# Optimization experiments

Measured on AMD Instinct MI355X. Metric: run time of the kernel, lower is better.

Reference implementation:

```python
import jax, jax.numpy as jnp
import numpy as np

FEATURES = 1024
NUM_HEADS = 16
HEAD_DIM = FEATURES // NUM_HEADS


def _cinit(key, shape):
    # complex_xavier_init from the source: std = sqrt(1/(fan_in + fan_out))
    fan_in = int(np.prod(shape[:-1]))
    fan_out = shape[-1]
    std = np.sqrt(1.0 / (fan_in + fan_out)).astype(np.float32)
    return jax.random.normal(key, shape, dtype=jnp.float32) * std


def setup_inputs() -> dict:
    key = jax.random.key(0)
    ks = jax.random.split(key, 12)
    B, S, F = 2, 2048, FEATURES
    inp = {
        'x_r': jax.random.normal(ks[0], (B, S, F), dtype=jnp.float32),
        'x_i': jax.random.normal(ks[1], (B, S, F), dtype=jnp.float32),
        'mask': jnp.ones((B, S), dtype=jnp.float32),
    }
    names = ['q', 'k', 'v', 'o']
    for idx, n in enumerate(names):
        inp[f'W{n}_r'] = _cinit(ks[2 + 2 * idx], (F, F))
        inp[f'W{n}_i'] = _cinit(ks[3 + 2 * idx], (F, F))
        inp[f'b{n}_r'] = jnp.zeros((F,), dtype=jnp.float32)
        inp[f'b{n}_i'] = jnp.zeros((F,), dtype=jnp.float32)
    return inp


def _complex_linear(xr, xi, Wr, Wi, br, bi):
    # (xr + i xi) @ (Wr + i Wi) + (br + i bi)
    yr = xr @ Wr - xi @ Wi + br
    yi = xr @ Wi + xi @ Wr + bi
    return yr, yi


def reference(x_r, x_i, mask,
              Wq_r, Wq_i, bq_r, bq_i,
              Wk_r, Wk_i, bk_r, bk_i,
              Wv_r, Wv_i, bv_r, bv_i,
              Wo_r, Wo_i, bo_r, bo_i):
    B, S, F = x_r.shape
    H, D = NUM_HEADS, HEAD_DIM

    Qr, Qi = _complex_linear(x_r, x_i, Wq_r, Wq_i, bq_r, bq_i)
    Kr, Ki = _complex_linear(x_r, x_i, Wk_r, Wk_i, bk_r, bk_i)
    Vr, Vi = _complex_linear(x_r, x_i, Wv_r, Wv_i, bv_r, bv_i)

    def split_heads(t):  # [B,S,F] -> [B,H,S,D]
        return t.reshape(B, S, H, D).transpose(0, 2, 1, 3)

    Qr, Qi, Kr, Ki, Vr, Vi = map(split_heads, (Qr, Qi, Kr, Ki, Vr, Vi))

    scale = 1.0 / jnp.sqrt(jnp.float32(D))
    # Re(Q K^H) = Qr.Kr + Qi.Ki
    scores = (jnp.einsum('bhqd,bhkd->bhqk', Qr, Kr)
              + jnp.einsum('bhqd,bhkd->bhqk', Qi, Ki)) * scale
    scores = scores + (1.0 - mask[:, None, None, :]) * -1e9
    attn = jax.nn.softmax(scores, axis=-1)  # real-valued weights

    out_r = jnp.einsum('bhqk,bhkd->bhqd', attn, Vr)
    out_i = jnp.einsum('bhqk,bhkd->bhqd', attn, Vi)

    def merge_heads(t):  # [B,H,S,D] -> [B,S,F]
        return t.transpose(0, 2, 1, 3).reshape(B, S, F)

    out_r, out_i = merge_heads(out_r), merge_heads(out_i)
    out_r, out_i = _complex_linear(out_r, out_i, Wo_r, Wo_i, bo_r, bo_i)
    # stack real/imag parts: [2, B, S, F]
    return jnp.stack([out_r, out_i], axis=0)
```

## Files before the change

kernel.cpp:

```cpp
#include <hip/hip_runtime.h>
#include <hip/hip_bf16.h>

typedef unsigned short u16;
typedef unsigned int   u32;
typedef __attribute__((ext_vector_type(8))) short bf16x8;
typedef __attribute__((ext_vector_type(4))) float f32x4;

#define FDIM 1024
#define NH   16
#define HD   64
#define SEQ  2048

#define MFMA16 __builtin_amdgcn_mfma_f32_16x16x32_bf16

__device__ __forceinline__ u16 f2bf(float f) {
    __hip_bfloat16 h = __float2bfloat16(f);
    return *reinterpret_cast<u16*>(&h);
}

__device__ __forceinline__ void g2l16(const u16* g, u16* l) {
    __builtin_amdgcn_global_load_lds(
        (const __attribute__((address_space(1))) unsigned int*)g,
        (__attribute__((address_space(3))) unsigned int*)l,
        16, 0, 0);
}

__global__ __launch_bounds__(256)
void convert_x(const float* __restrict__ xr, const float* __restrict__ xi,
               u16* __restrict__ dr, u16* __restrict__ di)
{
    const long n4 = (long)2 * SEQ * FDIM / 4;
    for (long i = (long)blockIdx.x * blockDim.x + threadIdx.x; i < n4;
         i += (long)gridDim.x * blockDim.x) {
        float4 v = ((const float4*)xr)[i];
        ushort4 o;
        o.x = f2bf(v.x); o.y = f2bf(v.y); o.z = f2bf(v.z); o.w = f2bf(v.w);
        ((ushort4*)dr)[i] = o;
        v = ((const float4*)xi)[i];
        o.x = f2bf(v.x); o.y = f2bf(v.y); o.z = f2bf(v.z); o.w = f2bf(v.w);
        ((ushort4*)di)[i] = o;
    }
}

__global__ __launch_bounds__(256)
void convert_w(const float* __restrict__ W0, const float* __restrict__ W1,
               const float* __restrict__ W2, const float* __restrict__ W3,
               const float* __restrict__ W4, const float* __restrict__ W5,
               const float* __restrict__ W6, const float* __restrict__ W7,
               u16* __restrict__ wt_base)
{
    __shared__ u16 T[64][68];
    const int z = blockIdx.z;
    const float* W = (z == 0) ? W0 : (z == 1) ? W1 : (z == 2) ? W2 : (z == 3) ? W3
                   : (z == 4) ? W4 : (z == 5) ? W5 : (z == 6) ? W6 : W7;
    u16* Wt = wt_base + (long)z * FDIM * FDIM;
    const int n0 = blockIdx.x * 64, k0 = blockIdx.y * 64;
    const int tid = threadIdx.x;
    const int cr = tid & 15, rr = tid >> 4;
    #pragma unroll
    for (int p = 0; p < 4; p++) {
        const int k = p * 16 + rr;
        float4 v = *(const float4*)&W[(long)(k0 + k) * FDIM + n0 + cr * 4];
        T[k][cr*4 + 0] = f2bf(v.x); T[k][cr*4 + 1] = f2bf(v.y);
        T[k][cr*4 + 2] = f2bf(v.z); T[k][cr*4 + 3] = f2bf(v.w);
    }
    __syncthreads();
    #pragma unroll
    for (int p = 0; p < 4; p++) {
        const int n = p * 16 + rr;
        ushort4 o;
        o.x = T[cr*4 + 0][n]; o.y = T[cr*4 + 1][n];
        o.z = T[cr*4 + 2][n]; o.w = T[cr*4 + 3][n];
        *(ushort4*)&Wt[(long)(n0 + n) * FDIM + k0 + cr*4] = o;
    }
}

__global__ __launch_bounds__(256, 3)
void proj_bf16(const u16* __restrict__ Xr_g, const u16* __restrict__ Xi_g,
               const u16* __restrict__ Wt_base,
               const float* __restrict__ bqr, const float* __restrict__ bqi,
               const float* __restrict__ bkr, const float* __restrict__ bki,
               const float* __restrict__ bvr, const float* __restrict__ bvi,
               u16* __restrict__ ws)
{
    __shared__ u16 XsR[2][64 * 32],  XsI[2][64 * 32];
    __shared__ u16 WsR[2][128 * 32], WsI[2][128 * 32];

    const int z = blockIdx.z, t = z % 3, b = z / 3;
    const u16* xr = Xr_g + (long)b * SEQ * FDIM;
    const u16* xi = Xi_g + (long)b * SEQ * FDIM;
    const long WT = (long)FDIM * FDIM;
    const u16* wr = Wt_base + (long)(2 * t) * WT;
    const u16* wi = wr + WT;
    const float* br = (t == 0) ? bqr : (t == 1) ? bkr : bvr;
    const float* bi = (t == 0) ? bqi : (t == 1) ? bki : bvi;
    const long TS = (long)2 * SEQ * FDIM;
    u16* outR = ws + (long)(t * 2) * TS + (long)b * SEQ * FDIM;
    u16* outI = outR + TS;

    const int tid = threadIdx.x;
    const int n0  = blockIdx.x * 128;
    const int m0  = blockIdx.y * 64;

    const int lane = tid & 63;
    const int wv   = tid >> 6;
    const int mwo  = (wv >> 1) * 32;
    const int nwo  = (wv & 1) * 64;
    const int ml   = lane & 15;
    const int kg   = lane >> 4;

    const int lr = lane >> 2;
    const int xc = (((lane & 3) ^ (lr & 3)) * 8);
    const int rc = ((kg ^ (ml & 3)) * 8);

    f32x4 accr[2][4], acci[2][4];
    #pragma unroll
    for (int i = 0; i < 2; i++)
        #pragma unroll
        for (int j = 0; j < 4; j++) { accr[i][j] = (f32x4)(0.0f); acci[i][j] = (f32x4)(0.0f); }

    #define PSTAGE(bufi, kk)                                                     \
        do {                                                                     \
            const int rsx  = wv * 16;                                            \
            const int rowx = rsx + lr;                                           \
            g2l16(xr + (long)(m0 + rowx) * FDIM + (kk) + xc, &XsR[bufi][rsx * 32]); \
            g2l16(xi + (long)(m0 + rowx) * FDIM + (kk) + xc, &XsI[bufi][rsx * 32]); \
            _Pragma("unroll")                                                    \
            for (int sub = 0; sub < 2; sub++) {                                  \
                const int rs  = wv * 32 + sub * 16;                              \
                const int row = rs + lr;                                         \
                g2l16(wr + (long)(n0 + row) * FDIM + (kk) + xc, &WsR[bufi][rs * 32]); \
                g2l16(wi + (long)(n0 + row) * FDIM + (kk) + xc, &WsI[bufi][rs * 32]); \
            }                                                                    \
        } while (0)

    int buf = 0;
    PSTAGE(0, 0);
    __syncthreads();

    for (int k0 = 0; k0 < FDIM; k0 += 32) {
        if (k0 + 32 < FDIM) PSTAGE(buf ^ 1, k0 + 32);

        bf16x8 ar[2], ai[2], nai[2], brf[4], bif[4];
        #pragma unroll
        for (int i = 0; i < 2; i++) {
            ar[i] = *(const bf16x8*)&XsR[buf][(mwo + 16*i + ml) * 32 + rc];
            union { bf16x8 v; u32 w[4]; } u;
            u.v = *(const bf16x8*)&XsI[buf][(mwo + 16*i + ml) * 32 + rc];
            ai[i] = u.v;
            u.w[0] ^= 0x80008000u; u.w[1] ^= 0x80008000u;
            u.w[2] ^= 0x80008000u; u.w[3] ^= 0x80008000u;
            nai[i] = u.v;
        }
        #pragma unroll
        for (int j = 0; j < 4; j++) {
            brf[j] = *(const bf16x8*)&WsR[buf][(nwo + 16*j + ml) * 32 + rc];
            bif[j] = *(const bf16x8*)&WsI[buf][(nwo + 16*j + ml) * 32 + rc];
        }
        #pragma unroll
        for (int i = 0; i < 2; i++)
            #pragma unroll
            for (int j = 0; j < 4; j++) {
                accr[i][j] = MFMA16(ar[i],  brf[j], accr[i][j], 0, 0, 0);
                accr[i][j] = MFMA16(nai[i], bif[j], accr[i][j], 0, 0, 0);
                acci[i][j] = MFMA16(ar[i],  bif[j], acci[i][j], 0, 0, 0);
                acci[i][j] = MFMA16(ai[i],  brf[j], acci[i][j], 0, 0, 0);
            }

        __syncthreads();
        buf ^= 1;
    }
    #undef PSTAGE

    #pragma unroll
    for (int j = 0; j < 4; j++) {
        const int n = n0 + nwo + 16*j + ml;
        const int hh = n >> 6, d = n & 63;
        const float bre = br[n];
        const float bim = bi[n];
        #pragma unroll
        for (int i = 0; i < 2; i++) {
            const int mb = m0 + mwo + 16*i + kg*4;
            if (t < 2) {
                #pragma unroll
                for (int r = 0; r < 4; r++) {
                    const long addr = ((long)hh * SEQ + (mb + r)) * HD + d;
                    outR[addr] = f2bf(accr[i][j][r] + bre);
                    outI[addr] = f2bf(acci[i][j][r] + bim);
                }
            } else {
                const long addr = ((long)hh * HD + d) * SEQ + mb;
                ushort4 vr, vi;
                vr.x = f2bf(accr[i][j][0] + bre); vr.y = f2bf(accr[i][j][1] + bre);
                vr.z = f2bf(accr[i][j][2] + bre); vr.w = f2bf(accr[i][j][3] + bre);
                vi.x = f2bf(acci[i][j][0] + bim); vi.y = f2bf(acci[i][j][1] + bim);
                vi.z = f2bf(acci[i][j][2] + bim); vi.w = f2bf(acci[i][j][3] + bim);
                *(ushort4*)&outR[addr] = vr;
                *(ushort4*)&outI[addr] = vi;
            }
        }
    }
}

__global__ __launch_bounds__(256, 4)
void attn_mfma(const u16* __restrict__ Qr_g, const u16* __restrict__ Qi_g,
               const u16* __restrict__ Kr_g, const u16* __restrict__ Ki_g,
               const u16* __restrict__ Vtr_g, const u16* __restrict__ Vti_g,
               const float* __restrict__ mask_g,
               u16* __restrict__ Ar_g, u16* __restrict__ Ai_g)
{
    __shared__ u16 KT[64 * 128];
    __shared__ u16 VT[128 * 64];

    const int tid  = threadIdx.x;
    const int lane = tid & 63;
    const int wv   = tid >> 6;
    const int ml   = lane & 15;
    const int quad = lane >> 4;

    const int L   = blockIdx.x + (blockIdx.y << 5) + (blockIdx.z << 9);
    const int xcd = L & 7, qq = L >> 3;
    const int q0  = (qq & 31) * 64;
    const int g   = ((qq >> 5) << 3) | xcd;
    const int h   = g & 15;
    const int b   = g >> 4;
    const long hb  = ((long)b * NH + h) * SEQ * HD;
    const float* mask = mask_g + (long)b * SEQ;

    bf16x8 qf[4];
    {
        const long row = hb + (long)(q0 + wv*16 + ml) * HD;
        qf[0] = *(const bf16x8*)(Qr_g + row + quad*8);
        qf[1] = *(const bf16x8*)(Qr_g + row + 32 + quad*8);
        qf[2] = *(const bf16x8*)(Qi_g + row + quad*8);
        qf[3] = *(const bf16x8*)(Qi_g + row + 32 + quad*8);
    }

    const u16* srcK[4];
    #pragma unroll
    for (int ii = 0; ii < 4; ii++) {
        const int rk = wv*16 + ii*4 + (lane >> 4);
        const int c  = (lane & 15) ^ (rk & 7);
        srcK[ii] = ((c < 8) ? Kr_g : Ki_g) + hb + (long)rk * HD + (c & 7) * 8;
    }
    const u16* srcV[4];
    #pragma unroll
    for (int jj = 0; jj < 4; jj++) {
        const int dv = wv*32 + jj*8 + (lane >> 3);
        const int c  = (lane & 7) ^ (dv & 7);
        srcV[jj] = ((dv < 64) ? Vtr_g : Vti_g) + hb + (long)(dv & 63) * SEQ + c * 8;
    }

    #define STAGE()                                                             \
        do {                                                                    \
            _Pragma("unroll")                                                   \
            for (int ii = 0; ii < 4; ii++)                                      \
                g2l16(srcK[ii], &KT[(wv*16 + ii*4) * 128]);                     \
            _Pragma("unroll")                                                   \
            for (int jj = 0; jj < 4; jj++)                                      \
                g2l16(srcV[jj], &VT[(wv*32 + jj*8) * 64]);                      \
            _Pragma("unroll")                                                   \
            for (int ii = 0; ii < 4; ii++) srcK[ii] += 64 * HD;                 \
            _Pragma("unroll")                                                   \
            for (int jj = 0; jj < 4; jj++) srcV[jj] += 64;                      \
        } while (0)

    f32x4 oacc[8];
    #pragma unroll
    for (int nt = 0; nt < 8; nt++) oacc[nt] = (f32x4)(0.0f);
    float m_run = -3.0e38f;
    float l_run = 0.0f;
    const float scale = 0.125f;

    const int NT = SEQ / 64;
    for (int t = 0; t < NT; ++t) {
        if (t) __syncthreads();
        STAGE();

        f32x4 mrow[4];
        #pragma unroll
        for (int mt = 0; mt < 4; mt++)
            mrow[mt] = *(const f32x4*)(mask + t*64 + mt*16 + quad*4);

        __syncthreads();

        f32x4 sacc[4];
        #pragma unroll
        for (int mt = 0; mt < 4; mt++) sacc[mt] = (f32x4)(0.0f);
        __builtin_amdgcn_s_setprio(1);
        #pragma unroll
        for (int mt = 0; mt < 4; mt++)
            #pragma unroll
            for (int kc = 0; kc < 4; kc++) {
                const bf16x8 kf = *(const bf16x8*)
                    &KT[(mt*16 + ml) * 128 + (((kc*4 + quad) ^ (ml & 7)) * 8)];
                sacc[mt] = MFMA16(kf, qf[kc], sacc[mt], 0, 0, 0);
            }
        __builtin_amdgcn_s_setprio(0);

        asm volatile("s_barrier" ::: "memory");

        u16* Pb = (u16*)&KT[0];
        float sv[4][4];
        #pragma unroll
        for (int mt = 0; mt < 4; mt++)
            #pragma unroll
            for (int r = 0; r < 4; r++)
                sv[mt][r] = sacc[mt][r] * scale + (1.0f - mrow[mt][r]) * -1.0e9f;

        float mA = fmaxf(fmaxf(sv[0][0], sv[0][1]), fmaxf(sv[0][2], sv[0][3]));
        float mB = fmaxf(fmaxf(sv[1][0], sv[1][1]), fmaxf(sv[1][2], sv[1][3]));
        float mC = fmaxf(fmaxf(sv[2][0], sv[2][1]), fmaxf(sv[2][2], sv[2][3]));
        float mD = fmaxf(fmaxf(sv[3][0], sv[3][1]), fmaxf(sv[3][2], sv[3][3]));
        float mx = fmaxf(fmaxf(mA, mB), fmaxf(mC, mD));
        mx = fmaxf(mx, __shfl_xor(mx, 16));
        mx = fmaxf(mx, __shfl_xor(mx, 32));
        const float mn = fmaxf(m_run, mx);
        const float al = __expf(m_run - mn);

        float p[4][4];
        #pragma unroll
        for (int mt = 0; mt < 4; mt++) {
            p[mt][0] = __expf(sv[mt][0] - mn);
            p[mt][1] = __expf(sv[mt][1] - mn);
            p[mt][2] = __expf(sv[mt][2] - mn);
            p[mt][3] = __expf(sv[mt][3] - mn);
        }
        const int qrow = wv*16 + ml;
        #pragma unroll
        for (int mt = 0; mt < 4; mt++) {
            ushort4 pb;
            pb.x = f2bf(p[mt][0]); pb.y = f2bf(p[mt][1]);
            pb.z = f2bf(p[mt][2]); pb.w = f2bf(p[mt][3]);
            *(ushort4*)&Pb[(long)qrow * 64
                           + (((mt*2 + (quad >> 1)) ^ (ml & 7)) * 8)
                           + (quad & 1) * 4] = pb;
        }
        float s0 = (p[0][0] + p[0][1]) + (p[0][2] + p[0][3]);
        float s1 = (p[1][0] + p[1][1]) + (p[1][2] + p[1][3]);
        float s2 = (p[2][0] + p[2][1]) + (p[2][2] + p[2][3]);
        float s3 = (p[3][0] + p[3][1]) + (p[3][2] + p[3][3]);
        float ps = (s0 + s1) + (s2 + s3);
        ps += __shfl_xor(ps, 16);
        ps += __shfl_xor(ps, 32);
        l_run = l_run * al + ps;
        m_run = mn;

        f32x4 al4;
        #pragma unroll
        for (int r = 0; r < 4; r++)
            al4[r] = __shfl(al, quad*20 + r);
        #pragma unroll
        for (int nt = 0; nt < 8; nt++) oacc[nt] *= al4;

        __builtin_amdgcn_s_setprio(1);
        #pragma unroll
        for (int kc = 0; kc < 2; kc++) {
            const int pchunk = ((kc*4 + quad) ^ (ml & 7)) * 8;
            const bf16x8 pf = *(const bf16x8*)&Pb[(long)qrow * 64 + pchunk];
            #pragma unroll
            for (int nt = 0; nt < 8; nt++) {
                const bf16x8 vf = *(const bf16x8*)
                    &VT[(nt*16 + ml) * 64 + (((kc*4 + quad) ^ (ml & 7)) * 8)];
                oacc[nt] = MFMA16(pf, vf, oacc[nt], 0, 0, 0);
            }
        }
        __builtin_amdgcn_s_setprio(0);
    }
    #undef STAGE

    const float linv = 1.0f / l_run;
    f32x4 li;
    #pragma unroll
    for (int r = 0; r < 4; r++)
        li[r] = __shfl(linv, quad*20 + r);
    const long abase = (long)b * SEQ * FDIM;
    #pragma unroll
    for (int nt = 0; nt < 8; nt++) {
        const int dim = nt*16 + ml;
        u16* dst = ((dim < 64) ? Ar_g : Ai_g) + abase
                 + (long)(q0 + wv*16 + quad*4) * FDIM + h * HD + (dim & 63);
        #pragma unroll
        for (int r = 0; r < 4; r++)
            dst[(long)r * FDIM] = f2bf(oacc[nt][r] * li[r]);
    }
}

__global__ __launch_bounds__(256, 3)
void oproj_bf16(const u16* __restrict__ Ar_all, const u16* __restrict__ Ai_all,
                const u16* __restrict__ Wtor,
                const float* __restrict__ bor, const float* __restrict__ boi,
                float* __restrict__ out)
{
    __shared__ u16 XsR[2][64 * 32],  XsI[2][64 * 32];
    __shared__ u16 WsR[2][128 * 32], WsI[2][128 * 32];

    const int b = blockIdx.z;
    const u16* ar = Ar_all + (long)b * SEQ * FDIM;
    const u16* ai = Ai_all + (long)b * SEQ * FDIM;
    const u16* wr = Wtor;
    const u16* wi = Wtor + (long)FDIM * FDIM;
    float* outR = out + (long)b * SEQ * FDIM;
    float* outI = out + (long)2 * SEQ * FDIM + (long)b * SEQ * FDIM;

    const int tid = threadIdx.x;
    const int n0  = blockIdx.x * 128;
    const int m0  = blockIdx.y * 64;

    const int lane = tid & 63;
    const int wv   = tid >> 6;
    const int mwo  = (wv >> 1) * 32;
    const int nwo  = (wv & 1) * 64;
    const int ml   = lane & 15;
    const int kg   = lane >> 4;

    const int lr = lane >> 2;
    const int xc = (((lane & 3) ^ (lr & 3)) * 8);
    const int rc = ((kg ^ (ml & 3)) * 8);

    f32x4 accr[2][4], acci[2][4];
    #pragma unroll
    for (int i = 0; i < 2; i++)
        #pragma unroll
        for (int j = 0; j < 4; j++) { accr[i][j] = (f32x4)(0.0f); acci[i][j] = (f32x4)(0.0f); }

    #define OSTAGE(bufi, kk)                                                     \
        do {                                                                     \
            const int rsx  = wv * 16;                                            \
            const int rowx = rsx + lr;                                           \
            g2l16(ar + (long)(m0 + rowx) * FDIM + (kk) + xc, &XsR[bufi][rsx * 32]); \
            g2l16(ai + (long)(m0 + rowx) * FDIM + (kk) + xc, &XsI[bufi][rsx * 32]); \
            _Pragma("unroll")                                                    \
            for (int sub = 0; sub < 2; sub++) {                                  \
                const int rs  = wv * 32 + sub * 16;                              \
                const int row = rs + lr;                                         \
                g2l16(wr + (long)(n0 + row) * FDIM + (kk) + xc, &WsR[bufi][rs * 32]); \
                g2l16(wi + (long)(n0 + row) * FDIM + (kk) + xc, &WsI[bufi][rs * 32]); \
            }                                                                    \
        } while (0)

    int buf = 0;
    OSTAGE(0, 0);
    __syncthreads();

    for (int k0 = 0; k0 < FDIM; k0 += 32) {
        if (k0 + 32 < FDIM) OSTAGE(buf ^ 1, k0 + 32);

        bf16x8 arf[2], aif[2], naif[2], brf[4], bif[4];
        #pragma unroll
        for (int i = 0; i < 2; i++) {
            arf[i] = *(const bf16x8*)&XsR[buf][(mwo + 16*i + ml) * 32 + rc];
            union { bf16x8 v; u32 w[4]; } u;
            u.v = *(const bf16x8*)&XsI[buf][(mwo + 16*i + ml) * 32 + rc];
            aif[i] = u.v;
            u.w[0] ^= 0x80008000u; u.w[1] ^= 0x80008000u;
            u.w[2] ^= 0x80008000u; u.w[3] ^= 0x80008000u;
            naif[i] = u.v;
        }
        #pragma unroll
        for (int j = 0; j < 4; j++) {
            brf[j] = *(const bf16x8*)&WsR[buf][(nwo + 16*j + ml) * 32 + rc];
            bif[j] = *(const bf16x8*)&WsI[buf][(nwo + 16*j + ml) * 32 + rc];
        }
        #pragma unroll
        for (int i = 0; i < 2; i++)
            #pragma unroll
            for (int j = 0; j < 4; j++) {
                accr[i][j] = MFMA16(arf[i],  brf[j], accr[i][j], 0, 0, 0);
                accr[i][j] = MFMA16(naif[i], bif[j], accr[i][j], 0, 0, 0);
                acci[i][j] = MFMA16(arf[i],  bif[j], acci[i][j], 0, 0, 0);
                acci[i][j] = MFMA16(aif[i],  brf[j], acci[i][j], 0, 0, 0);
            }

        __syncthreads();
        buf ^= 1;
    }
    #undef OSTAGE

    #pragma unroll
    for (int j = 0; j < 4; j++) {
        const int n = n0 + nwo + 16*j + ml;
        const float bre = bor[n];
        const float bim = boi[n];
        #pragma unroll
        for (int i = 0; i < 2; i++) {
            #pragma unroll
            for (int r = 0; r < 4; r++) {
                const int m = m0 + mwo + 16*i + kg*4 + r;
                const long addr = (long)m * FDIM + n;
                outR[addr] = accr[i][j][r] + bre;
                outI[addr] = acci[i][j][r] + bim;
            }
        }
    }
}

extern "C" void kernel_launch(void* const* d_in, const int* in_sizes, int n_in,
                              void* d_out, int out_size, void* d_ws, size_t ws_size,
                              hipStream_t stream)
{
    const float* x_r  = (const float*)d_in[0];
    const float* x_i  = (const float*)d_in[1];
    const float* mask = (const float*)d_in[2];
    const float *Wq_r = (const float*)d_in[3],  *Wq_i = (const float*)d_in[4];
    const float *bq_r = (const float*)d_in[5],  *bq_i = (const float*)d_in[6];
    const float *Wk_r = (const float*)d_in[7],  *Wk_i = (const float*)d_in[8];
    const float *bk_r = (const float*)d_in[9],  *bk_i = (const float*)d_in[10];
    const float *Wv_r = (const float*)d_in[11], *Wv_i = (const float*)d_in[12];
    const float *bv_r = (const float*)d_in[13], *bv_i = (const float*)d_in[14];
    const float *Wo_r = (const float*)d_in[15], *Wo_i = (const float*)d_in[16];
    const float *bo_r = (const float*)d_in[17], *bo_i = (const float*)d_in[18];

    u16* ws = (u16*)d_ws;
    const long TS = (long)2 * SEQ * FDIM;
    const long WT = (long)FDIM * FDIM;
    u16 *Qr = ws,          *Qi = ws + TS;
    u16 *Kr = ws + 2*TS,   *Ki = ws + 3*TS;
    u16 *Vtr = ws + 4*TS,  *Vti = ws + 5*TS;
    u16 *Ar = ws + 6*TS,   *Ai = ws + 7*TS;
    u16 *Xbr = Ar,         *Xbi = Ai;
    u16 *Wt  = ws + 8*TS;

    convert_x<<<dim3(2048), 256, 0, stream>>>(x_r, x_i, Xbr, Xbi);
    convert_w<<<dim3(16, 16, 8), 256, 0, stream>>>(Wq_r, Wq_i, Wk_r, Wk_i,
                                                   Wv_r, Wv_i, Wo_r, Wo_i, Wt);

    proj_bf16<<<dim3(8, 32, 6), 256, 0, stream>>>(Xbr, Xbi, Wt,
        bq_r, bq_i, bk_r, bk_i, bv_r, bv_i, ws);

    attn_mfma<<<dim3(SEQ / 64, NH, 2), 256, 0, stream>>>(Qr, Qi, Kr, Ki, Vtr, Vti,
                                                         mask, Ar, Ai);

    oproj_bf16<<<dim3(8, 32, 2), 256, 0, stream>>>(Ar, Ai, Wt + 6*WT,
                                                   bo_r, bo_i, (float*)d_out);
}
```

Before: 392.8 us.

## Shrink projection tiles, remap blocks across XCDs, and use exp2 softmax with lazy rescale

The projection and output-projection GEMMs drop from 64x128 to 64x64 tiles, which doubles the grid, raises the occupancy hint to 4, and remaps block IDs so neighbouring N tiles land on the same XCD for L2 reuse. The attention softmax folds log2(e) into the scale, calls v_exp_f32 directly, and skips the accumulator rescale when no row max grows anywhere in the wave. Smaller tiles cut per-block data reuse and raise total global and LDS traffic, in exchange for more parallelism and better cache locality.

```diff
diff --git a/kernel.cpp b/kernel.cpp
--- a/kernel.cpp
+++ b/kernel.cpp
@@ -23,6 +23,12 @@
         (const __attribute__((address_space(1))) unsigned int*)g,
         (__attribute__((address_space(3))) unsigned int*)l,
         16, 0, 0);
+}
+
+__device__ __forceinline__ float exp2v(float x) {
+    float d;
+    asm("v_exp_f32 %0, %1" : "=v"(d) : "v"(x));
+    return d;
 }
 
 __global__ __launch_bounds__(256)
@@ -75,7 +81,7 @@
     }
 }
 
-__global__ __launch_bounds__(256, 3)
+__global__ __launch_bounds__(256, 4)
 void proj_bf16(const u16* __restrict__ Xr_g, const u16* __restrict__ Xi_g,
                const u16* __restrict__ Wt_base,
                const float* __restrict__ bqr, const float* __restrict__ bqi,
@@ -83,10 +89,19 @@
                const float* __restrict__ bvr, const float* __restrict__ bvi,
                u16* __restrict__ ws)
 {
-    __shared__ u16 XsR[2][64 * 32],  XsI[2][64 * 32];
-    __shared__ u16 WsR[2][128 * 32], WsI[2][128 * 32];
-
-    const int z = blockIdx.z, t = z % 3, b = z / 3;
+    __shared__ u16 XsR[2][64 * 32], XsI[2][64 * 32];
+    __shared__ u16 WsR[2][64 * 32], WsI[2][64 * 32];
+
+    const int L   = blockIdx.x + (blockIdx.y << 4) + (blockIdx.z << 9);
+    const int xcd = L & 7;
+    const int qq  = L >> 3;
+    const int y   = qq & 31;
+    const int gg  = qq >> 5;
+    const int gid = gg * 8 + xcd;
+    const int x   = gid & 15;
+    const int zz  = gid >> 4;
+    const int t = zz % 3, b = zz / 3;
+
     const u16* xr = Xr_g + (long)b * SEQ * FDIM;
     const u16* xi = Xi_g + (long)b * SEQ * FDIM;
     const long WT = (long)FDIM * FDIM;
@@ -99,13 +114,13 @@
     u16* outI = outR + TS;
 
     const int tid = threadIdx.x;
-    const int n0  = blockIdx.x * 128;
-    const int m0  = blockIdx.y * 64;
+    const int n0  = x * 64;
+    const int m0  = y * 64;
 
     const int lane = tid & 63;
     const int wv   = tid >> 6;
     const int mwo  = (wv >> 1) * 32;
-    const int nwo  = (wv & 1) * 64;
+    const int nwo  = (wv & 1) * 32;
     const int ml   = lane & 15;
     const int kg   = lane >> 4;
 
@@ -113,11 +128,11 @@
     const int xc = (((lane & 3) ^ (lr & 3)) * 8);
     const int rc = ((kg ^ (ml & 3)) * 8);
 
-    f32x4 accr[2][4], acci[2][4];
+    f32x4 accr[2][2], acci[2][2];
     #pragma unroll
     for (int i = 0; i < 2; i++)
         #pragma unroll
-        for (int j = 0; j < 4; j++) { accr[i][j] = (f32x4)(0.0f); acci[i][j] = (f32x4)(0.0f); }
+        for (int j = 0; j < 2; j++) { accr[i][j] = (f32x4)(0.0f); acci[i][j] = (f32x4)(0.0f); }
 
     #define PSTAGE(bufi, kk)                                                     \
         do {                                                                     \
@@ -125,13 +140,8 @@
             const int rowx = rsx + lr;                                           \
             g2l16(xr + (long)(m0 + rowx) * FDIM + (kk) + xc, &XsR[bufi][rsx * 32]); \
             g2l16(xi + (long)(m0 + rowx) * FDIM + (kk) + xc, &XsI[bufi][rsx * 32]); \
-            _Pragma("unroll")                                                    \
-            for (int sub = 0; sub < 2; sub++) {                                  \
-                const int rs  = wv * 32 + sub * 16;                              \
-                const int row = rs + lr;                                         \
-                g2l16(wr + (long)(n0 + row) * FDIM + (kk) + xc, &WsR[bufi][rs * 32]); \
-                g2l16(wi + (long)(n0 + row) * FDIM + (kk) + xc, &WsI[bufi][rs * 32]); \
-            }                                                                    \
+            g2l16(wr + (long)(n0 + rowx) * FDIM + (kk) + xc, &WsR[bufi][rsx * 32]); \
+            g2l16(wi + (long)(n0 + rowx) * FDIM + (kk) + xc, &WsI[bufi][rsx * 32]); \
         } while (0)
 
     int buf = 0;
@@ -141,7 +151,7 @@
     for (int k0 = 0; k0 < FDIM; k0 += 32) {
         if (k0 + 32 < FDIM) PSTAGE(buf ^ 1, k0 + 32);
 
-        bf16x8 ar[2], ai[2], nai[2], brf[4], bif[4];
+        bf16x8 ar[2], ai[2], nai[2], brf[2], bif[2];
         #pragma unroll
         for (int i = 0; i < 2; i++) {
             ar[i] = *(const bf16x8*)&XsR[buf][(mwo + 16*i + ml) * 32 + rc];
@@ -153,14 +163,14 @@
             nai[i] = u.v;
         }
         #pragma unroll
-        for (int j = 0; j < 4; j++) {
+        for (int j = 0; j < 2; j++) {
             brf[j] = *(const bf16x8*)&WsR[buf][(nwo + 16*j + ml) * 32 + rc];
             bif[j] = *(const bf16x8*)&WsI[buf][(nwo + 16*j + ml) * 32 + rc];
         }
         #pragma unroll
         for (int i = 0; i < 2; i++)
             #pragma unroll
-            for (int j = 0; j < 4; j++) {
+            for (int j = 0; j < 2; j++) {
                 accr[i][j] = MFMA16(ar[i],  brf[j], accr[i][j], 0, 0, 0);
                 accr[i][j] = MFMA16(nai[i], bif[j], accr[i][j], 0, 0, 0);
                 acci[i][j] = MFMA16(ar[i],  bif[j], acci[i][j], 0, 0, 0);
@@ -173,7 +183,7 @@
     #undef PSTAGE
 
     #pragma unroll
-    for (int j = 0; j < 4; j++) {
+    for (int j = 0; j < 2; j++) {
         const int n = n0 + nwo + 16*j + ml;
         const int hh = n >> 6, d = n & 63;
         const float bre = br[n];
@@ -270,7 +280,8 @@
     for (int nt = 0; nt < 8; nt++) oacc[nt] = (f32x4)(0.0f);
     float m_run = -3.0e38f;
     float l_run = 0.0f;
-    const float scale = 0.125f;
+    const float SCALE2 = 0.125f * 1.44269504088896f;
+    const float MC     = -1.44269504e9f;
 
     const int NT = SEQ / 64;
     for (int t = 0; t < NT; ++t) {
@@ -306,25 +317,28 @@
         for (int mt = 0; mt < 4; mt++)
             #pragma unroll
             for (int r = 0; r < 4; r++)
-                sv[mt][r] = sacc[mt][r] * scale + (1.0f - mrow[mt][r]) * -1.0e9f;
+                sv[mt][r] = sacc[mt][r] * SCALE2 + (1.0f - mrow[mt][r]) * MC;
 
         float mA = fmaxf(fmaxf(sv[0][0], sv[0][1]), fmaxf(sv[0][2], sv[0][3]));
         float mB = fmaxf(fmaxf(sv[1][0], sv[1][1]), fmaxf(sv[1][2], sv[1][3]));
-        float mC = fmaxf(fmaxf(sv[2][0], sv[2][1]), fmaxf(sv[2][2], sv[2][3]));
+        float mC2 = fmaxf(fmaxf(sv[2][0], sv[2][1]), fmaxf(sv[2][2], sv[2][3]));
         float mD = fmaxf(fmaxf(sv[3][0], sv[3][1]), fmaxf(sv[3][2], sv[3][3]));
-        float mx = fmaxf(fmaxf(mA, mB), fmaxf(mC, mD));
+        float mx = fmaxf(fmaxf(mA, mB), fmaxf(mC2, mD));
         mx = fmaxf(mx, __shfl_xor(mx, 16));
         mx = fmaxf(mx, __shfl_xor(mx, 32));
-        const float mn = fmaxf(m_run, mx);
-        const float al = __expf(m_run - mn);
+
+        const int grow = __any(mx > m_run);
+        float mn, al;
+        if (grow) { mn = fmaxf(m_run, mx); al = exp2v(m_run - mn); }
+        else      { mn = m_run;            al = 1.0f; }
 
         float p[4][4];
         #pragma unroll
         for (int mt = 0; mt < 4; mt++) {
-            p[mt][0] = __expf(sv[mt][0] - mn);
-            p[mt][1] = __expf(sv[mt][1] - mn);
-            p[mt][2] = __expf(sv[mt][2] - mn);
-            p[mt][3] = __expf(sv[mt][3] - mn);
+            p[mt][0] = exp2v(sv[mt][0] - mn);
+            p[mt][1] = exp2v(sv[mt][1] - mn);
+            p[mt][2] = exp2v(sv[mt][2] - mn);
+            p[mt][3] = exp2v(sv[mt][3] - mn);
         }
         const int qrow = wv*16 + ml;
         #pragma unroll
@@ -343,15 +357,18 @@
         float ps = (s0 + s1) + (s2 + s3);
         ps += __shfl_xor(ps, 16);
         ps += __shfl_xor(ps, 32);
-        l_run = l_run * al + ps;
+        if (grow) {
+            l_run = l_run * al + ps;
+            f32x4 al4;
+            #pragma unroll
+            for (int r = 0; r < 4; r++)
+                al4[r] = __shfl(al, quad*20 + r);
+            #pragma unroll
+            for (int nt = 0; nt < 8; nt++) oacc[nt] *= al4;
+        } else {
+            l_run += ps;
+        }
         m_run = mn;
-
-        f32x4 al4;
-        #pragma unroll
-        for (int r = 0; r < 4; r++)
-            al4[r] = __shfl(al, quad*20 + r);
-        #pragma unroll
-        for (int nt = 0; nt < 8; nt++) oacc[nt] *= al4;
 
         __builtin_amdgcn_s_setprio(1);
         #pragma unroll
@@ -386,16 +403,24 @@
     }
 }
 
-__global__ __launch_bounds__(256, 3)
+__global__ __launch_bounds__(256, 4)
 void oproj_bf16(const u16* __restrict__ Ar_all, const u16* __restrict__ Ai_all,
                 const u16* __restrict__ Wtor,
                 const float* __restrict__ bor, const float* __restrict__ boi,
                 float* __restrict__ out)
 {
-    __shared__ u16 XsR[2][64 * 32],  XsI[2][64 * 32];
-    __shared__ u16 WsR[2][128 * 32], WsI[2][128 * 32];
-
-    const int b = blockIdx.z;
+    __shared__ u16 XsR[2][64 * 32], XsI[2][64 * 32];
+    __shared__ u16 WsR[2][64 * 32], WsI[2][64 * 32];
+
+    const int L   = blockIdx.x + (blockIdx.y << 4) + (blockIdx.z << 9);
+    const int xcd = L & 7;
+    const int qq  = L >> 3;
+    const int y   = qq & 31;
+    const int gg  = qq >> 5;
+    const int gid = gg * 8 + xcd;
+    const int x   = gid & 15;
+    const int b   = gid >> 4;
+
     const u16* ar = Ar_all + (long)b * SEQ * FDIM;
     const u16* ai = Ai_all + (long)b * SEQ * FDIM;
     const u16* wr = Wtor;
@@ -404,13 +429,13 @@
     float* outI = out + (long)2 * SEQ * FDIM + (long)b * SEQ * FDIM;
 
     const int tid = threadIdx.x;
-    const int n0  = blockIdx.x * 128;
-    const int m0  = blockIdx.y * 64;
+    const int n0  = x * 64;
+    const int m0  = y * 64;
 
     const int lane = tid & 63;
     const int wv   = tid >> 6;
     const int mwo  = (wv >> 1) * 32;
-    const int nwo  = (wv & 1) * 64;
+    const int nwo  = (wv & 1) * 32;
     const int ml   = lane & 15;
     const int kg   = lane >> 4;
 
@@ -418,11 +443,11 @@
     const int xc = (((lane & 3) ^ (lr & 3)) * 8);
     const int rc = ((kg ^ (ml & 3)) * 8);
 
-    f32x4 accr[2][4], acci[2][4];
+    f32x4 accr[2][2], acci[2][2];
     #pragma unroll
     for (int i = 0; i < 2; i++)
         #pragma unroll
-        for (int j = 0; j < 4; j++) { accr[i][j] = (f32x4)(0.0f); acci[i][j] = (f32x4)(0.0f); }
+        for (int j = 0; j < 2; j++) { accr[i][j] = (f32x4)(0.0f); acci[i][j] = (f32x4)(0.0f); }
 
     #define OSTAGE(bufi, kk)                                                     \
         do {                                                                     \
@@ -430,13 +455,8 @@
             const int rowx = rsx + lr;                                           \
             g2l16(ar + (long)(m0 + rowx) * FDIM + (kk) + xc, &XsR[bufi][rsx * 32]); \
             g2l16(ai + (long)(m0 + rowx) * FDIM + (kk) + xc, &XsI[bufi][rsx * 32]); \
-            _Pragma("unroll")                                                    \
-            for (int sub = 0; sub < 2; sub++) {                                  \
-                const int rs  = wv * 32 + sub * 16;                              \
-                const int row = rs + lr;                                         \
-                g2l16(wr + (long)(n0 + row) * FDIM + (kk) + xc, &WsR[bufi][rs * 32]); \
-                g2l16(wi + (long)(n0 + row) * FDIM + (kk) + xc, &WsI[bufi][rs * 32]); \
-            }                                                                    \
+            g2l16(wr + (long)(n0 + rowx) * FDIM + (kk) + xc, &WsR[bufi][rsx * 32]); \
+            g2l16(wi + (long)(n0 + rowx) * FDIM + (kk) + xc, &WsI[bufi][rsx * 32]); \
         } while (0)
 
     int buf = 0;
@@ -446,7 +466,7 @@
     for (int k0 = 0; k0 < FDIM; k0 += 32) {
         if (k0 + 32 < FDIM) OSTAGE(buf ^ 1, k0 + 32);
 
-        bf16x8 arf[2], aif[2], naif[2], brf[4], bif[4];
+        bf16x8 arf[2], aif[2], naif[2], brf[2], bif[2];
         #pragma unroll
         for (int i = 0; i < 2; i++) {
             arf[i] = *(const bf16x8*)&XsR[buf][(mwo + 16*i + ml) * 32 + rc];
@@ -458,14 +478,14 @@
             naif[i] = u.v;
         }
         #pragma unroll
-        for (int j = 0; j < 4; j++) {
+        for (int j = 0; j < 2; j++) {
             brf[j] = *(const bf16x8*)&WsR[buf][(nwo + 16*j + ml) * 32 + rc];
             bif[j] = *(const bf16x8*)&WsI[buf][(nwo + 16*j + ml) * 32 + rc];
         }
         #pragma unroll
         for (int i = 0; i < 2; i++)
             #pragma unroll
-            for (int j = 0; j < 4; j++) {
+            for (int j = 0; j < 2; j++) {
                 accr[i][j] = MFMA16(arf[i],  brf[j], accr[i][j], 0, 0, 0);
                 accr[i][j] = MFMA16(naif[i], bif[j], accr[i][j], 0, 0, 0);
                 acci[i][j] = MFMA16(arf[i],  bif[j], acci[i][j], 0, 0, 0);
@@ -478,7 +498,7 @@
     #undef OSTAGE
 
     #pragma unroll
-    for (int j = 0; j < 4; j++) {
+    for (int j = 0; j < 2; j++) {
         const int n = n0 + nwo + 16*j + ml;
         const float bre = bor[n];
         const float bim = boi[n];
@@ -525,12 +545,12 @@
     convert_w<<<dim3(16, 16, 8), 256, 0, stream>>>(Wq_r, Wq_i, Wk_r, Wk_i,
                                                    Wv_r, Wv_i, Wo_r, Wo_i, Wt);
 
-    proj_bf16<<<dim3(8, 32, 6), 256, 0, stream>>>(Xbr, Xbi, Wt,
+    proj_bf16<<<dim3(16, 32, 6), 256, 0, stream>>>(Xbr, Xbi, Wt,
         bq_r, bq_i, bk_r, bk_i, bv_r, bv_i, ws);
 
     attn_mfma<<<dim3(SEQ / 64, NH, 2), 256, 0, stream>>>(Qr, Qi, Kr, Ki, Vtr, Vti,
                                                          mask, Ar, Ai);
 
-    oproj_bf16<<<dim3(8, 32, 2), 256, 0, stream>>>(Ar, Ai, Wt + 6*WT,
-                                                   bo_r, bo_i, (float*)d_out);
-}
+    oproj_bf16<<<dim3(16, 32, 2), 256, 0, stream>>>(Ar, Ai, Wt + 6*WT,
+                                                    bo_r, bo_i, (float*)d_out);
+}
```

After: 398.9 us. Within noise of the previous version (+1.5%).

## Remap projection blocks per XCD and use exp2 with conditional rescale in attention

Applied to the files above, without the earlier changes.

The projection and output-projection GEMMs now remap the linear block index so that blocks sharing the same weight column tile land on the same XCD, aiming to improve L2 reuse of weights. The attention softmax folds log2(e) into the scale and mask constant and calls the hardware v_exp_f32 directly instead of __expf. It also skips the accumulator rescale and its shuffles when no row maximum grew in the wavefront. The remapping assumes the grid is exactly 8 x 32 x Z with round-robin XCD dispatch, and the wave-uniform branch adds a little control flow.

```diff
diff --git a/kernel.cpp b/kernel.cpp
--- a/kernel.cpp
+++ b/kernel.cpp
@@ -23,6 +23,12 @@
         (const __attribute__((address_space(1))) unsigned int*)g,
         (__attribute__((address_space(3))) unsigned int*)l,
         16, 0, 0);
+}
+
+__device__ __forceinline__ float exp2v(float x) {
+    float d;
+    asm("v_exp_f32 %0, %1" : "=v"(d) : "v"(x));
+    return d;
 }
 
 __global__ __launch_bounds__(256)
@@ -86,7 +92,16 @@
     __shared__ u16 XsR[2][64 * 32],  XsI[2][64 * 32];
     __shared__ u16 WsR[2][128 * 32], WsI[2][128 * 32];
 
-    const int z = blockIdx.z, t = z % 3, b = z / 3;
+    const int L   = blockIdx.x + (blockIdx.y << 3) + (blockIdx.z << 8);
+    const int xcd = L & 7;
+    const int qq  = L >> 3;
+    const int y   = qq & 31;
+    const int gg  = qq >> 5;
+    const int gid = gg * 8 + xcd;
+    const int x   = gid & 7;
+    const int z   = gid >> 3;
+    const int t = z % 3, b = z / 3;
+
     const u16* xr = Xr_g + (long)b * SEQ * FDIM;
     const u16* xi = Xi_g + (long)b * SEQ * FDIM;
     const long WT = (long)FDIM * FDIM;
@@ -99,8 +114,8 @@
     u16* outI = outR + TS;
 
     const int tid = threadIdx.x;
-    const int n0  = blockIdx.x * 128;
-    const int m0  = blockIdx.y * 64;
+    const int n0  = x * 128;
+    const int m0  = y * 64;
 
     const int lane = tid & 63;
     const int wv   = tid >> 6;
@@ -270,7 +285,8 @@
     for (int nt = 0; nt < 8; nt++) oacc[nt] = (f32x4)(0.0f);
     float m_run = -3.0e38f;
     float l_run = 0.0f;
-    const float scale = 0.125f;
+    const float SCALE2 = 0.125f * 1.44269504088896f;
+    const float MC     = -1.44269504e9f;
 
     const int NT = SEQ / 64;
     for (int t = 0; t < NT; ++t) {
@@ -306,25 +322,28 @@
         for (int mt = 0; mt < 4; mt++)
             #pragma unroll
             for (int r = 0; r < 4; r++)
-                sv[mt][r] = sacc[mt][r] * scale + (1.0f - mrow[mt][r]) * -1.0e9f;
+                sv[mt][r] = sacc[mt][r] * SCALE2 + (1.0f - mrow[mt][r]) * MC;
 
         float mA = fmaxf(fmaxf(sv[0][0], sv[0][1]), fmaxf(sv[0][2], sv[0][3]));
         float mB = fmaxf(fmaxf(sv[1][0], sv[1][1]), fmaxf(sv[1][2], sv[1][3]));
-        float mC = fmaxf(fmaxf(sv[2][0], sv[2][1]), fmaxf(sv[2][2], sv[2][3]));
+        float mC2 = fmaxf(fmaxf(sv[2][0], sv[2][1]), fmaxf(sv[2][2], sv[2][3]));
         float mD = fmaxf(fmaxf(sv[3][0], sv[3][1]), fmaxf(sv[3][2], sv[3][3]));
-        float mx = fmaxf(fmaxf(mA, mB), fmaxf(mC, mD));
+        float mx = fmaxf(fmaxf(mA, mB), fmaxf(mC2, mD));
         mx = fmaxf(mx, __shfl_xor(mx, 16));
         mx = fmaxf(mx, __shfl_xor(mx, 32));
-        const float mn = fmaxf(m_run, mx);
-        const float al = __expf(m_run - mn);
+
+        const int grow = __any(mx > m_run);
+        float mn, al;
+        if (grow) { mn = fmaxf(m_run, mx); al = exp2v(m_run - mn); }
+        else      { mn = m_run;            al = 1.0f; }
 
         float p[4][4];
         #pragma unroll
         for (int mt = 0; mt < 4; mt++) {
-            p[mt][0] = __expf(sv[mt][0] - mn);
-            p[mt][1] = __expf(sv[mt][1] - mn);
-            p[mt][2] = __expf(sv[mt][2] - mn);
-            p[mt][3] = __expf(sv[mt][3] - mn);
+            p[mt][0] = exp2v(sv[mt][0] - mn);
+            p[mt][1] = exp2v(sv[mt][1] - mn);
+            p[mt][2] = exp2v(sv[mt][2] - mn);
+            p[mt][3] = exp2v(sv[mt][3] - mn);
         }
         const int qrow = wv*16 + ml;
         #pragma unroll
@@ -343,15 +362,18 @@
         float ps = (s0 + s1) + (s2 + s3);
         ps += __shfl_xor(ps, 16);
         ps += __shfl_xor(ps, 32);
-        l_run = l_run * al + ps;
+        if (grow) {
+            l_run = l_run * al + ps;
+            f32x4 al4;
+            #pragma unroll
+            for (int r = 0; r < 4; r++)
+                al4[r] = __shfl(al, quad*20 + r);
+            #pragma unroll
+            for (int nt = 0; nt < 8; nt++) oacc[nt] *= al4;
+        } else {
+            l_run += ps;
+        }
         m_run = mn;
-
-        f32x4 al4;
-        #pragma unroll
-        for (int r = 0; r < 4; r++)
-            al4[r] = __shfl(al, quad*20 + r);
-        #pragma unroll
-        for (int nt = 0; nt < 8; nt++) oacc[nt] *= al4;
 
         __builtin_amdgcn_s_setprio(1);
         #pragma unroll
@@ -395,7 +417,15 @@
     __shared__ u16 XsR[2][64 * 32],  XsI[2][64 * 32];
     __shared__ u16 WsR[2][128 * 32], WsI[2][128 * 32];
 
-    const int b = blockIdx.z;
+    const int L   = blockIdx.x + (blockIdx.y << 3) + (blockIdx.z << 8);
+    const int xcd = L & 7;
+    const int qq  = L >> 3;
+    const int y   = qq & 31;
+    const int gg  = qq >> 5;
+    const int gid = gg * 8 + xcd;
+    const int x   = gid & 7;
+    const int b   = gid >> 3;
+
     const u16* ar = Ar_all + (long)b * SEQ * FDIM;
     const u16* ai = Ai_all + (long)b * SEQ * FDIM;
     const u16* wr = Wtor;
@@ -404,8 +434,8 @@
     float* outI = out + (long)2 * SEQ * FDIM + (long)b * SEQ * FDIM;
 
     const int tid = threadIdx.x;
-    const int n0  = blockIdx.x * 128;
-    const int m0  = blockIdx.y * 64;
+    const int n0  = x * 128;
+    const int m0  = y * 64;
 
     const int lane = tid & 63;
     const int wv   = tid >> 6;
```

After: 403.8 us. 2.8% more time.
